# Kernel optimization log

Measured on AMD Instinct MI355X. Metric: run time of the kernel, lower is better.

Reference implementation:

```python
import jax, jax.numpy as jnp
import numpy as np

EPS = 1e-5

def _ln(x, g, b):
    mu = jnp.mean(x, axis=-1, keepdims=True)
    var = jnp.mean((x - mu) ** 2, axis=-1, keepdims=True)
    return (x - mu) / jnp.sqrt(var + EPS) * g + b

def setup_inputs() -> dict:
    key = jax.random.key(0)
    ks = jax.random.split(key, 8)
    S, B, L, M, D, Nq, H = 4, 256, 256, 4, 512, 4, 2048
    G = (M + 2) * D
    inp = {
        'ns_tokens': jax.random.normal(ks[0], (B, M, D), jnp.float32),
        'seq_tokens': jax.random.normal(ks[1], (S, B, L, D), jnp.float32),
        'seq_padding_masks': jax.random.randint(ks[2], (S, B, L), 0, 2).astype(bool),
        'seq_stats': jax.random.normal(ks[3], (S, B, 6), jnp.float32),
        'gin_gamma': jnp.ones((G,), jnp.float32),
        'gin_beta': jnp.zeros((G,), jnp.float32),
        'stat_W': 0.02 * jax.random.normal(ks[4], (S, 6, D), jnp.float32),
        'stat_b': jnp.zeros((S, D), jnp.float32),
        'stat_ln_g': jnp.ones((S, D), jnp.float32),
        'stat_ln_b': jnp.zeros((S, D), jnp.float32),
        'W1': 0.02 * jax.random.normal(ks[5], (S, Nq, G, H), jnp.float32),
        'b1': jnp.zeros((S, Nq, H), jnp.float32),
        'W2': 0.02 * jax.random.normal(ks[6], (S, Nq, H, D), jnp.float32),
        'b2': jnp.zeros((S, Nq, D), jnp.float32),
        'ln_g': jnp.ones((S, Nq, D), jnp.float32),
        'ln_b': jnp.zeros((S, Nq, D), jnp.float32),
    }
    return inp

def reference(ns_tokens, seq_tokens, seq_padding_masks, seq_stats,
              gin_gamma, gin_beta, stat_W, stat_b, stat_ln_g, stat_ln_b,
              W1, b1, W2, b2, ln_g, ln_b):
    S, B = seq_tokens.shape[0], ns_tokens.shape[0]
    ns_flat = ns_tokens.reshape(B, -1)                       # (B, M*D)
    valid = (~seq_padding_masks).astype(seq_tokens.dtype)[..., None]  # (S,B,L,1)
    denom = jnp.clip(jnp.sum(valid, axis=2), 1.0)            # (S,B,1)
    pooled = jnp.sum(seq_tokens * valid, axis=2) / denom     # (S,B,D)
    stat = jnp.einsum('sbf,sfd->sbd', seq_stats, stat_W) + stat_b[:, None]
    stat = _ln(stat, stat_ln_g[:, None], stat_ln_b[:, None])  # (S,B,D)
    gi = jnp.concatenate([jnp.broadcast_to(ns_flat[None], (S, B, ns_flat.shape[1])), pooled, stat], axis=-1)
    gi = _ln(gi, gin_gamma, gin_beta)                        # (S,B,G)
    h = jax.nn.silu(jnp.einsum('sbg,sqgh->sqbh', gi, W1) + b1[:, :, None])
    q = jnp.einsum('sqbh,sqhd->sqbd', h, W2) + b2[:, :, None]
    q = _ln(q, ln_g[:, :, None], ln_b[:, :, None])           # (S,Nq,B,D)
    return jnp.transpose(q, (0, 2, 1, 3))                    # (S,B,Nq,D)
```

## Files before the change

### kernel.cpp

```cpp
#include <hip/hip_runtime.h>
#include <hip/hip_bf16.h>

#define S_ 4
#define B_ 256
#define L_ 256
#define D_ 512
#define NQ_ 4
#define H_ 2048
#define G_ 3072

typedef __attribute__((ext_vector_type(4))) float f32x4;
typedef __attribute__((ext_vector_type(8))) short s16x8;

__device__ __forceinline__ unsigned short f2bf(float x) {
    __hip_bfloat16 hb = __float2bfloat16(x);
    return reinterpret_cast<unsigned short&>(hb);
}

__device__ __forceinline__ void gll16(const void* g, void* l) {
    __builtin_amdgcn_global_load_lds(
        (const __attribute__((address_space(1))) unsigned int*)g,
        (__attribute__((address_space(3))) unsigned int*)l, 16, 0, 0);
}

__device__ __forceinline__ float block_sum256(float v, float* red) {
    #pragma unroll
    for (int off = 32; off > 0; off >>= 1) v += __shfl_down(v, off, 64);
    int tid = threadIdx.x;
    int lane = tid & 63, wid = tid >> 6;
    if (lane == 0) red[wid] = v;
    __syncthreads();
    float r = (tid < 4) ? red[tid] : 0.f;
    #pragma unroll
    for (int off = 4; off > 0; off >>= 1) r += __shfl_down(r, off, 64);
    if (tid == 0) red[0] = r;
    __syncthreads();
    float out = red[0];
    __syncthreads();
    return out;
}

__global__ __launch_bounds__(256) void pool_kernel(
    const float* __restrict__ seq_tokens,
    const unsigned char* __restrict__ masks_raw,
    float* __restrict__ pooled)
{
    const int sb = blockIdx.x;
    const int tid = threadIdx.x;
    __shared__ float sval[L_];
    __shared__ float scount[4];
    __shared__ f32x4 spart[256];
    __shared__ int is_bool_flag;

    if (tid == 0) is_bool_flag = 0;
    __syncthreads();
    {
        unsigned int w = reinterpret_cast<const unsigned int*>(masks_raw)[tid];
        if (w & 0xFFFFFF00u) is_bool_flag = 1;
    }
    __syncthreads();
    const bool is_bool = (is_bool_flag != 0);

    int mval;
    if (is_bool) mval = masks_raw[(size_t)sb * L_ + tid];
    else         mval = reinterpret_cast<const int*>(masks_raw)[(size_t)sb * L_ + tid];
    float valid = mval ? 0.f : 1.f;
    sval[tid] = valid;
    float c = valid;
    #pragma unroll
    for (int off = 32; off > 0; off >>= 1) c += __shfl_down(c, off, 64);
    if ((tid & 63) == 0) scount[tid >> 6] = c;
    __syncthreads();
    const float denom = fmaxf(scount[0] + scount[1] + scount[2] + scount[3], 1.f);

    const float* base = seq_tokens + (size_t)sb * L_ * D_;
    const int cidx = tid & 127;
    const int rg = tid >> 7;
    f32x4 acc = {0.f, 0.f, 0.f, 0.f};
    for (int l = rg; l < L_; l += 2) {
        float vl = sval[l];
        f32x4 v = *reinterpret_cast<const f32x4*>(base + (size_t)l * D_ + cidx * 4);
        acc += v * vl;
    }
    spart[tid] = acc;
    __syncthreads();
    if (tid < 128) {
        f32x4 r = spart[tid] + spart[tid + 128];
        r *= (1.f / denom);
        *reinterpret_cast<f32x4*>(pooled + (size_t)sb * D_ + cidx * 4) = r;
    }
}

__global__ __launch_bounds__(256) void gi_kernel(
    const float* __restrict__ ns_tokens,
    const float* __restrict__ seq_stats,
    const float* __restrict__ stat_W,
    const float* __restrict__ stat_b,
    const float* __restrict__ stat_ln_g,
    const float* __restrict__ stat_ln_b,
    const float* __restrict__ gin_gamma,
    const float* __restrict__ gin_beta,
    const float* __restrict__ pooled,
    __hip_bfloat16* __restrict__ gi)
{
    const int sb = blockIdx.x;
    const int s = sb >> 8;
    const int b = sb & 255;
    const int tid = threadIdx.x;
    __shared__ float red[8];
    __shared__ float sstat[D_];

    float st[6];
    #pragma unroll
    for (int f = 0; f < 6; ++f) st[f] = seq_stats[(size_t)sb * 6 + f];

    float sp[2];
    #pragma unroll
    for (int k = 0; k < 2; ++k) {
        int d = tid + k * 256;
        float a = stat_b[s * D_ + d];
        #pragma unroll
        for (int f = 0; f < 6; ++f) a += st[f] * stat_W[(s * 6 + f) * D_ + d];
        sp[k] = a;
    }
    float ssum = block_sum256(sp[0] + sp[1], red);
    float ssq  = block_sum256(sp[0] * sp[0] + sp[1] * sp[1], red);
    float mu = ssum / D_;
    float var = ssq / D_ - mu * mu;
    float rinv = rsqrtf(var + 1e-5f);
    #pragma unroll
    for (int k = 0; k < 2; ++k) {
        int d = tid + k * 256;
        sstat[d] = (sp[k] - mu) * rinv * stat_ln_g[s * D_ + d] + stat_ln_b[s * D_ + d];
    }
    __syncthreads();

    float gv[12];
    float gsum = 0.f, gsq = 0.f;
    #pragma unroll
    for (int k = 0; k < 12; ++k) {
        int g = tid + k * 256;
        float v;
        if (g < 2048)       v = ns_tokens[(size_t)b * 2048 + g];
        else if (g < 2560)  v = pooled[(size_t)sb * D_ + (g - 2048)];
        else                v = sstat[g - 2560];
        gv[k] = v;
        gsum += v;
        gsq += v * v;
    }
    gsum = block_sum256(gsum, red);
    gsq  = block_sum256(gsq, red);
    mu = gsum / G_;
    var = gsq / G_ - mu * mu;
    rinv = rsqrtf(var + 1e-5f);
    #pragma unroll
    for (int k = 0; k < 12; ++k) {
        int g = tid + k * 256;
        float o = (gv[k] - mu) * rinv * gin_gamma[g] + gin_beta[g];
        gi[(size_t)sb * G_ + g] = __float2bfloat16(o);
    }
}

__global__ __launch_bounds__(256) void gemm1_kernel(
    const __hip_bfloat16* __restrict__ gi,
    const float* __restrict__ W1,
    const float* __restrict__ b1,
    __hip_bfloat16* __restrict__ hbuf)
{
    const int bid = blockIdx.x;
    const int wg = (bid & 7) * 64 + (bid >> 3);
    const int ntile = wg & 31;
    const int sq = wg >> 5;
    const int s = sq >> 2;
    const int tid = threadIdx.x;
    const int lane = tid & 63;
    const int wid = tid >> 6;

    __shared__ __align__(16) unsigned short As[2][256 * 64];
    __shared__ __align__(16) unsigned short Ws[2][64 * 64];

    const char* Ag = reinterpret_cast<const char*>(gi + (size_t)s * B_ * G_);
    const float* Wb = W1 + (size_t)sq * G_ * H_ + ntile * 64;

    f32x4 acc[4][4];
    #pragma unroll
    for (int i = 0; i < 4; ++i)
        #pragma unroll
        for (int j = 0; j < 4; ++j) acc[i][j] = (f32x4){0.f, 0.f, 0.f, 0.f};

    unsigned aoff[8];
    #pragma unroll
    for (int i = 0; i < 8; ++i) {
        int row = wid * 64 + i * 8 + (lane >> 3);
        int swz = ((lane >> 3) ^ i) & 7;
        aoff[i] = (unsigned)row * (G_ * 2) + (((lane & 7) ^ swz) * 16);
    }

    const int wn0 = (tid & 15) * 4;
    const int wk0 = (tid >> 4) * 4;
    unsigned offW[4];
    #pragma unroll
    for (int nn = 0; nn < 4; ++nn) {
        int row = wn0 + nn;
        int swz = (row ^ (row >> 3)) & 7;
        offW[nn] = (unsigned)((row * 128 + wk0 * 2) ^ (swz << 4));
    }

    unsigned offA[2][4], offB[2][4];
    #pragma unroll
    for (int kb = 0; kb < 2; ++kb) {
        #pragma unroll
        for (int mi = 0; mi < 4; ++mi) {
            int r = wid * 64 + mi * 16 + (lane & 15);
            int swz = (r ^ (r >> 3)) & 7;
            offA[kb][mi] = r * 128 + ((((lane >> 4) + kb * 4) ^ swz) * 16);
        }
        #pragma unroll
        for (int ni = 0; ni < 4; ++ni) {
            int r = ni * 16 + (lane & 15);
            int swz = (r ^ (r >> 3)) & 7;
            offB[kb][ni] = r * 128 + ((((lane >> 4) + kb * 4) ^ swz) * 16);
        }
    }

    {
        char* dst = reinterpret_cast<char*>(&As[0][0]);
        #pragma unroll
        for (int i = 0; i < 8; ++i)
            gll16(Ag + aoff[i], dst + (wid * 64 + i * 8) * 128);
        f32x4 w0[4];
        #pragma unroll
        for (int kk = 0; kk < 4; ++kk)
            w0[kk] = *reinterpret_cast<const f32x4*>(Wb + (size_t)(wk0 + kk) * H_ + wn0);
        #pragma unroll
        for (int nn = 0; nn < 4; ++nn) {
            unsigned long long pk =
                (unsigned long long)f2bf(w0[0][nn]) |
                ((unsigned long long)f2bf(w0[1][nn]) << 16) |
                ((unsigned long long)f2bf(w0[2][nn]) << 32) |
                ((unsigned long long)f2bf(w0[3][nn]) << 48);
            *reinterpret_cast<unsigned long long*>(reinterpret_cast<char*>(&Ws[0][0]) + offW[nn]) = pk;
        }
        asm volatile("s_waitcnt lgkmcnt(0)" ::: "memory");
        __builtin_amdgcn_s_barrier();
    }

    for (int kt = 0; kt < G_ / 64; ++kt) {
        const int cur = kt & 1, nxt = cur ^ 1;
        const int kn = (kt < G_ / 64 - 1) ? kt + 1 : G_ / 64 - 1;

        f32x4 wreg[4];
        {
            const float* wp = Wb + (size_t)(kn * 64 + wk0) * H_ + wn0;
            #pragma unroll
            for (int kk = 0; kk < 4; ++kk)
                wreg[kk] = *reinterpret_cast<const f32x4*>(wp + (size_t)kk * H_);
        }
        {
            char* dst = reinterpret_cast<char*>(&As[nxt][0]);
            const unsigned kbyte = (unsigned)kn * 128;
            #pragma unroll
            for (int i = 0; i < 8; ++i)
                gll16(Ag + (aoff[i] + kbyte), dst + (wid * 64 + i * 8) * 128);
        }
        asm volatile("s_waitcnt vmcnt(12)" ::: "memory");
        __builtin_amdgcn_sched_barrier(0);

        const char* Al = reinterpret_cast<const char*>(&As[cur][0]);
        const char* Wl = reinterpret_cast<const char*>(&Ws[cur][0]);
        #pragma unroll
        for (int kb = 0; kb < 2; ++kb) {
            s16x8 af[4], bfr[4];
            #pragma unroll
            for (int mi = 0; mi < 4; ++mi)
                af[mi] = *reinterpret_cast<const s16x8*>(Al + offA[kb][mi]);
            #pragma unroll
            for (int ni = 0; ni < 4; ++ni)
                bfr[ni] = *reinterpret_cast<const s16x8*>(Wl + offB[kb][ni]);
            #pragma unroll
            for (int mi = 0; mi < 4; ++mi)
                #pragma unroll
                for (int ni = 0; ni < 4; ++ni)
                    acc[mi][ni] = __builtin_amdgcn_mfma_f32_16x16x32_bf16(af[mi], bfr[ni], acc[mi][ni], 0, 0, 0);
        }

        #pragma unroll
        for (int nn = 0; nn < 4; ++nn) {
            unsigned long long pk =
                (unsigned long long)f2bf(wreg[0][nn]) |
                ((unsigned long long)f2bf(wreg[1][nn]) << 16) |
                ((unsigned long long)f2bf(wreg[2][nn]) << 32) |
                ((unsigned long long)f2bf(wreg[3][nn]) << 48);
            *reinterpret_cast<unsigned long long*>(reinterpret_cast<char*>(&Ws[nxt][0]) + offW[nn]) = pk;
        }
        asm volatile("s_waitcnt lgkmcnt(0)" ::: "memory");
        __builtin_amdgcn_s_barrier();
    }

    const float* b1p = b1 + (size_t)sq * H_ + ntile * 64;
    __hip_bfloat16* hp = hbuf + (size_t)sq * B_ * H_;
    #pragma unroll
    for (int mi = 0; mi < 4; ++mi)
        #pragma unroll
        for (int ni = 0; ni < 4; ++ni)
            #pragma unroll
            for (int r = 0; r < 4; ++r) {
                int row = wid * 64 + mi * 16 + ((lane >> 4) << 2) + r;
                int coll = ni * 16 + (lane & 15);
                float x = acc[mi][ni][r] + b1p[coll];
                float sg = 1.f / (1.f + __expf(-x));
                hp[(size_t)row * H_ + ntile * 64 + coll] = __float2bfloat16(x * sg);
            }
}

__global__ __launch_bounds__(256) void gemm2_kernel(
    const __hip_bfloat16* __restrict__ hbuf,
    const float* __restrict__ W2,
    __hip_bfloat16* __restrict__ qpre)
{
    const int bid = blockIdx.x;
    const int wg = (bid & 7) * 32 + (bid >> 3);
    const int ntile = wg & 7;
    const int mtile = (wg >> 3) & 1;
    const int sq = wg >> 4;
    const int tid = threadIdx.x;
    const int lane = tid & 63;
    const int wid = tid >> 6;
    const int wm = wid >> 1, wn = wid & 1;

    __shared__ __align__(16) unsigned short As[128 * 64];
    __shared__ __align__(16) unsigned short Ws[64 * 64];

    const __hip_bfloat16* Ab = hbuf + ((size_t)sq * B_ + mtile * 128) * H_;
    const float* Wb = W2 + (size_t)sq * H_ * D_ + ntile * 64;

    f32x4 acc[4][2];
    #pragma unroll
    for (int i = 0; i < 4; ++i)
        #pragma unroll
        for (int j = 0; j < 2; ++j) acc[i][j] = (f32x4){0.f, 0.f, 0.f, 0.f};

    const int wn0 = (tid & 15) * 4;
    const int wk0 = (tid >> 4) * 4;

    for (int kt = 0; kt < H_ / 64; ++kt) {
        const int kbase = kt * 64;
        __syncthreads();
        float wv[4][4];
        #pragma unroll
        for (int kk = 0; kk < 4; ++kk) {
            f32x4 t = *reinterpret_cast<const f32x4*>(Wb + (size_t)(kbase + wk0 + kk) * D_ + wn0);
            #pragma unroll
            for (int j = 0; j < 4; ++j) wv[kk][j] = t[j];
        }
        #pragma unroll
        for (int i = 0; i < 4; ++i) {
            int slot = i * 256 + tid;
            int row = slot >> 3, cc = slot & 7;
            int swz = (row ^ (row >> 3)) & 7;
            s16x8 v = *reinterpret_cast<const s16x8*>(Ab + (size_t)row * H_ + kbase + cc * 8);
            *reinterpret_cast<s16x8*>(&As[row * 64 + ((cc ^ swz) * 8)]) = v;
        }
        #pragma unroll
        for (int nn = 0; nn < 4; ++nn) {
            int row = wn0 + nn;
            int swz = (row ^ (row >> 3)) & 7;
            unsigned long long pk =
                (unsigned long long)f2bf(wv[0][nn]) |
                ((unsigned long long)f2bf(wv[1][nn]) << 16) |
                ((unsigned long long)f2bf(wv[2][nn]) << 32) |
                ((unsigned long long)f2bf(wv[3][nn]) << 48);
            int byteoff = (row * 128 + wk0 * 2) ^ (swz << 4);
            *reinterpret_cast<unsigned long long*>(reinterpret_cast<char*>(Ws) + byteoff) = pk;
        }
        __syncthreads();
        #pragma unroll
        for (int kb = 0; kb < 2; ++kb) {
            s16x8 af[4], bfr[2];
            #pragma unroll
            for (int mi = 0; mi < 4; ++mi) {
                int r = wm * 64 + mi * 16 + (lane & 15);
                int swz = (r ^ (r >> 3)) & 7;
                int chunk = ((lane >> 4) + kb * 4) ^ swz;
                af[mi] = *reinterpret_cast<const s16x8*>(&As[r * 64 + chunk * 8]);
            }
            #pragma unroll
            for (int ni = 0; ni < 2; ++ni) {
                int r = wn * 32 + ni * 16 + (lane & 15);
                int swz = (r ^ (r >> 3)) & 7;
                int chunk = ((lane >> 4) + kb * 4) ^ swz;
                bfr[ni] = *reinterpret_cast<const s16x8*>(&Ws[r * 64 + chunk * 8]);
            }
            #pragma unroll
            for (int mi = 0; mi < 4; ++mi)
                #pragma unroll
                for (int ni = 0; ni < 2; ++ni)
                    acc[mi][ni] = __builtin_amdgcn_mfma_f32_16x16x32_bf16(af[mi], bfr[ni], acc[mi][ni], 0, 0, 0);
        }
    }
    #pragma unroll
    for (int mi = 0; mi < 4; ++mi)
        #pragma unroll
        for (int ni = 0; ni < 2; ++ni)
            #pragma unroll
            for (int r = 0; r < 4; ++r) {
                int row = mtile * 128 + wm * 64 + mi * 16 + ((lane >> 4) << 2) + r;
                int col = ntile * 64 + wn * 32 + ni * 16 + (lane & 15);
                qpre[((size_t)sq * B_ + row) * D_ + col] = __float2bfloat16(acc[mi][ni][r]);
            }
}

__global__ __launch_bounds__(256) void lnout_kernel(
    const __hip_bfloat16* __restrict__ qpre,
    const float* __restrict__ b2,
    const float* __restrict__ lng,
    const float* __restrict__ lnb,
    float* __restrict__ out)
{
    const int idx = blockIdx.x;
    const int sq = idx >> 8;
    const int b = idx & 255;
    const int tid = threadIdx.x;
    __shared__ float red[8];

    float v[2];
    #pragma unroll
    for (int k = 0; k < 2; ++k) {
        int d = tid + k * 256;
        v[k] = __bfloat162float(qpre[(size_t)idx * D_ + d]) + b2[sq * D_ + d];
    }
    float sum = block_sum256(v[0] + v[1], red);
    float sq2 = block_sum256(v[0] * v[0] + v[1] * v[1], red);
    float mu = sum / D_;
    float var = sq2 / D_ - mu * mu;
    float rinv = rsqrtf(var + 1e-5f);
    const int s = sq >> 2, q = sq & 3;
    #pragma unroll
    for (int k = 0; k < 2; ++k) {
        int d = tid + k * 256;
        float o = (v[k] - mu) * rinv * lng[sq * D_ + d] + lnb[sq * D_ + d];
        out[(((size_t)s * B_ + b) * NQ_ + q) * D_ + d] = o;
    }
}

extern "C" void kernel_launch(void* const* d_in, const int* in_sizes, int n_in,
                              void* d_out, int out_size, void* d_ws, size_t ws_size,
                              hipStream_t stream) {
    const float* ns_tokens   = (const float*)d_in[0];
    const float* seq_tokens  = (const float*)d_in[1];
    const unsigned char* masks = (const unsigned char*)d_in[2];
    const float* seq_stats   = (const float*)d_in[3];
    const float* gin_gamma   = (const float*)d_in[4];
    const float* gin_beta    = (const float*)d_in[5];
    const float* stat_W      = (const float*)d_in[6];
    const float* stat_b      = (const float*)d_in[7];
    const float* stat_ln_g   = (const float*)d_in[8];
    const float* stat_ln_b   = (const float*)d_in[9];
    const float* W1          = (const float*)d_in[10];
    const float* b1          = (const float*)d_in[11];
    const float* W2          = (const float*)d_in[12];
    const float* b2          = (const float*)d_in[13];
    const float* ln_g        = (const float*)d_in[14];
    const float* ln_b        = (const float*)d_in[15];
    float* out = (float*)d_out;

    char* ws = (char*)d_ws;
    float* pooled        = (float*)(ws);
    __hip_bfloat16* gi   = (__hip_bfloat16*)(ws + 2097152);
    __hip_bfloat16* hbuf = (__hip_bfloat16*)(ws + 2097152 + 6291456);
    __hip_bfloat16* qpre = (__hip_bfloat16*)(ws + 2097152 + 6291456 + 16777216);

    pool_kernel<<<dim3(S_ * B_), dim3(256), 0, stream>>>(seq_tokens, masks, pooled);
    gi_kernel<<<dim3(S_ * B_), dim3(256), 0, stream>>>(ns_tokens, seq_stats, stat_W, stat_b,
                                                       stat_ln_g, stat_ln_b, gin_gamma, gin_beta,
                                                       pooled, gi);
    gemm1_kernel<<<dim3(32 * S_ * NQ_), dim3(256), 0, stream>>>(gi, W1, b1, hbuf);
    gemm2_kernel<<<dim3(2 * D_ / 64 * S_ * NQ_), dim3(256), 0, stream>>>(hbuf, W2, qpre);
    lnout_kernel<<<dim3(S_ * NQ_ * B_), dim3(256), 0, stream>>>(qpre, b2, ln_g, ln_b, out);
}
```

Measured before the change: 268.8 us.

## Prefetch W1 fp32 tiles two k-steps ahead with register double-buffering in gemm1

The gemm1 main loop now holds two register sets for the fp32 W1 tile and issues the global load for tile k+2 while tile k+1 is converted to bf16 and written to LDS before the MFMAs. The loop is unrolled by two with a macro so the register roles alternate. This is meant to hide the global-memory latency of the W1 stream, which previously had only one iteration of slack. In exchange, each thread holds sixteen more registers, which may reduce occupancy, and the LDS conversion store now sits before the MFMA block instead of after it.

```diff
diff --git a/kernel.cpp b/kernel.cpp
--- a/kernel.cpp
+++ b/kernel.cpp
@@ -161,6 +161,55 @@
     }
 }
 
+#define G1_BODY(KT, CUR, NXT, WP, WQ)                                                  \
+  {                                                                                    \
+    const int kn2 = ((KT) < 46) ? (KT) + 2 : 47;                                       \
+    const float* wp_ = Wb + (size_t)(kn2 * 64 + wk0) * H_ + wn0;                       \
+    _Pragma("unroll")                                                                  \
+    for (int kk = 0; kk < 4; ++kk)                                                     \
+        WQ[kk] = *reinterpret_cast<const f32x4*>(wp_ + (size_t)kk * H_);               \
+    {                                                                                  \
+        const int kn1 = ((KT) < 47) ? (KT) + 1 : 47;                                   \
+        char* dst = reinterpret_cast<char*>(&As[NXT][0]);                              \
+        const unsigned kbyte = (unsigned)kn1 * 128;                                    \
+        _Pragma("unroll")                                                              \
+        for (int i = 0; i < 8; ++i)                                                    \
+            gll16(Ag + (aoff[i] + kbyte), dst + (wid * 64 + i * 8) * 128);             \
+    }                                                                                  \
+    asm volatile("s_waitcnt vmcnt(12)" ::: "memory");                                  \
+    __builtin_amdgcn_sched_barrier(0);                                                 \
+    _Pragma("unroll")                                                                  \
+    for (int nn = 0; nn < 4; ++nn) {                                                   \
+        unsigned long long pk =                                                        \
+            (unsigned long long)f2bf(WP[0][nn]) |                                      \
+            ((unsigned long long)f2bf(WP[1][nn]) << 16) |                              \
+            ((unsigned long long)f2bf(WP[2][nn]) << 32) |                              \
+            ((unsigned long long)f2bf(WP[3][nn]) << 48);                               \
+        *reinterpret_cast<unsigned long long*>(                                        \
+            reinterpret_cast<char*>(&Ws[NXT][0]) + offW[nn]) = pk;                     \
+    }                                                                                  \
+    const char* Al = reinterpret_cast<const char*>(&As[CUR][0]);                       \
+    const char* Wl = reinterpret_cast<const char*>(&Ws[CUR][0]);                       \
+    _Pragma("unroll")                                                                  \
+    for (int kb = 0; kb < 2; ++kb) {                                                   \
+        s16x8 af[4], bfr[4];                                                           \
+        _Pragma("unroll")                                                              \
+        for (int mi = 0; mi < 4; ++mi)                                                 \
+            af[mi] = *reinterpret_cast<const s16x8*>(Al + offA[kb][mi]);               \
+        _Pragma("unroll")                                                              \
+        for (int ni = 0; ni < 4; ++ni)                                                 \
+            bfr[ni] = *reinterpret_cast<const s16x8*>(Wl + offB[kb][ni]);              \
+        _Pragma("unroll")                                                              \
+        for (int mi = 0; mi < 4; ++mi)                                                 \
+            _Pragma("unroll")                                                          \
+            for (int ni = 0; ni < 4; ++ni)                                             \
+                acc[mi][ni] = __builtin_amdgcn_mfma_f32_16x16x32_bf16(                 \
+                    af[mi], bfr[ni], acc[mi][ni], 0, 0, 0);                            \
+    }                                                                                  \
+    asm volatile("s_waitcnt lgkmcnt(0)" ::: "memory");                                 \
+    __builtin_amdgcn_s_barrier();                                                      \
+  }
+
 __global__ __launch_bounds__(256) void gemm1_kernel(
     const __hip_bfloat16* __restrict__ gi,
     const float* __restrict__ W1,
@@ -223,78 +272,38 @@
         }
     }
 
+    f32x4 wA[4], wB[4];
+
     {
         char* dst = reinterpret_cast<char*>(&As[0][0]);
         #pragma unroll
         for (int i = 0; i < 8; ++i)
             gll16(Ag + aoff[i], dst + (wid * 64 + i * 8) * 128);
-        f32x4 w0[4];
         #pragma unroll
         for (int kk = 0; kk < 4; ++kk)
-            w0[kk] = *reinterpret_cast<const f32x4*>(Wb + (size_t)(wk0 + kk) * H_ + wn0);
+            wA[kk] = *reinterpret_cast<const f32x4*>(Wb + (size_t)(wk0 + kk) * H_ + wn0);
+        const float* wp1 = Wb + (size_t)(64 + wk0) * H_ + wn0;
+        #pragma unroll
+        for (int kk = 0; kk < 4; ++kk)
+            wB[kk] = *reinterpret_cast<const f32x4*>(wp1 + (size_t)kk * H_);
+        asm volatile("s_waitcnt vmcnt(4)" ::: "memory");
+        __builtin_amdgcn_sched_barrier(0);
         #pragma unroll
         for (int nn = 0; nn < 4; ++nn) {
             unsigned long long pk =
-                (unsigned long long)f2bf(w0[0][nn]) |
-                ((unsigned long long)f2bf(w0[1][nn]) << 16) |
-                ((unsigned long long)f2bf(w0[2][nn]) << 32) |
-                ((unsigned long long)f2bf(w0[3][nn]) << 48);
+                (unsigned long long)f2bf(wA[0][nn]) |
+                ((unsigned long long)f2bf(wA[1][nn]) << 16) |
+                ((unsigned long long)f2bf(wA[2][nn]) << 32) |
+                ((unsigned long long)f2bf(wA[3][nn]) << 48);
             *reinterpret_cast<unsigned long long*>(reinterpret_cast<char*>(&Ws[0][0]) + offW[nn]) = pk;
         }
         asm volatile("s_waitcnt lgkmcnt(0)" ::: "memory");
         __builtin_amdgcn_s_barrier();
     }
 
-    for (int kt = 0; kt < G_ / 64; ++kt) {
-        const int cur = kt & 1, nxt = cur ^ 1;
-        const int kn = (kt < G_ / 64 - 1) ? kt + 1 : G_ / 64 - 1;
-
-        f32x4 wreg[4];
-        {
-            const float* wp = Wb + (size_t)(kn * 64 + wk0) * H_ + wn0;
-            #pragma unroll
-            for (int kk = 0; kk < 4; ++kk)
-                wreg[kk] = *reinterpret_cast<const f32x4*>(wp + (size_t)kk * H_);
-        }
-        {
-            char* dst = reinterpret_cast<char*>(&As[nxt][0]);
-            const unsigned kbyte = (unsigned)kn * 128;
-            #pragma unroll
-            for (int i = 0; i < 8; ++i)
-                gll16(Ag + (aoff[i] + kbyte), dst + (wid * 64 + i * 8) * 128);
-        }
-        asm volatile("s_waitcnt vmcnt(12)" ::: "memory");
-        __builtin_amdgcn_sched_barrier(0);
-
-        const char* Al = reinterpret_cast<const char*>(&As[cur][0]);
-        const char* Wl = reinterpret_cast<const char*>(&Ws[cur][0]);
-        #pragma unroll
-        for (int kb = 0; kb < 2; ++kb) {
-            s16x8 af[4], bfr[4];
-            #pragma unroll
-            for (int mi = 0; mi < 4; ++mi)
-                af[mi] = *reinterpret_cast<const s16x8*>(Al + offA[kb][mi]);
-            #pragma unroll
-            for (int ni = 0; ni < 4; ++ni)
-                bfr[ni] = *reinterpret_cast<const s16x8*>(Wl + offB[kb][ni]);
-            #pragma unroll
-            for (int mi = 0; mi < 4; ++mi)
-                #pragma unroll
-                for (int ni = 0; ni < 4; ++ni)
-                    acc[mi][ni] = __builtin_amdgcn_mfma_f32_16x16x32_bf16(af[mi], bfr[ni], acc[mi][ni], 0, 0, 0);
-        }
-
-        #pragma unroll
-        for (int nn = 0; nn < 4; ++nn) {
-            unsigned long long pk =
-                (unsigned long long)f2bf(wreg[0][nn]) |
-                ((unsigned long long)f2bf(wreg[1][nn]) << 16) |
-                ((unsigned long long)f2bf(wreg[2][nn]) << 32) |
-                ((unsigned long long)f2bf(wreg[3][nn]) << 48);
-            *reinterpret_cast<unsigned long long*>(reinterpret_cast<char*>(&Ws[nxt][0]) + offW[nn]) = pk;
-        }
-        asm volatile("s_waitcnt lgkmcnt(0)" ::: "memory");
-        __builtin_amdgcn_s_barrier();
+    for (int kt = 0; kt < 48; kt += 2) {
+        G1_BODY(kt,     0, 1, wB, wA);
+        G1_BODY(kt + 1, 1, 0, wA, wB);
     }
 
     const float* b1p = b1 + (size_t)sq * H_ + ntile * 64;
```

After: 310.6 us. 1.16x slower.

## Double-buffer gemm2 with async LDS loads and narrower N tiles for more blocks

Applied to the files above, without the earlier changes.

Rewrites the second GEMM so the hbuf tile goes straight from global memory into LDS with global_load_lds into a double buffer. The next W2 tile is loaded into registers while the current tile runs MFMAs, and only one barrier is taken per K step. The N tile shrinks from 64 to 32 columns, doubling the grid to 512 blocks for better CU coverage, and launch bounds request 4 blocks per CU. The cost is that each block reuses less A data, so hbuf is read from global memory twice as often, and correctness now depends on the hand-written waitcnt placement.

```diff
diff --git a/kernel.cpp b/kernel.cpp
--- a/kernel.cpp
+++ b/kernel.cpp
@@ -313,99 +313,141 @@
             }
 }
 
-__global__ __launch_bounds__(256) void gemm2_kernel(
+__global__ __launch_bounds__(256, 4) void gemm2_kernel(
     const __hip_bfloat16* __restrict__ hbuf,
     const float* __restrict__ W2,
     __hip_bfloat16* __restrict__ qpre)
 {
     const int bid = blockIdx.x;
-    const int wg = (bid & 7) * 32 + (bid >> 3);
-    const int ntile = wg & 7;
-    const int mtile = (wg >> 3) & 1;
-    const int sq = wg >> 4;
+    const int wg = (bid & 7) * 64 + (bid >> 3);
+    const int ntile = wg & 15;
+    const int mtile = (wg >> 4) & 1;
+    const int sq = wg >> 5;
     const int tid = threadIdx.x;
     const int lane = tid & 63;
     const int wid = tid >> 6;
-    const int wm = wid >> 1, wn = wid & 1;
-
-    __shared__ __align__(16) unsigned short As[128 * 64];
-    __shared__ __align__(16) unsigned short Ws[64 * 64];
-
-    const __hip_bfloat16* Ab = hbuf + ((size_t)sq * B_ + mtile * 128) * H_;
-    const float* Wb = W2 + (size_t)sq * H_ * D_ + ntile * 64;
-
-    f32x4 acc[4][2];
-    #pragma unroll
-    for (int i = 0; i < 4; ++i)
+
+    __shared__ __align__(16) unsigned short As[2][128 * 64];
+    __shared__ __align__(16) unsigned short Ws[2][32 * 64];
+
+    const char* Ag = reinterpret_cast<const char*>(hbuf + ((size_t)sq * B_ + mtile * 128) * H_);
+    const float* Wb = W2 + (size_t)sq * H_ * D_ + ntile * 32;
+
+    f32x4 acc[2][2];
+    #pragma unroll
+    for (int i = 0; i < 2; ++i)
         #pragma unroll
         for (int j = 0; j < 2; ++j) acc[i][j] = (f32x4){0.f, 0.f, 0.f, 0.f};
 
-    const int wn0 = (tid & 15) * 4;
-    const int wk0 = (tid >> 4) * 4;
+    unsigned aoff[4];
+    #pragma unroll
+    for (int i = 0; i < 4; ++i) {
+        int row = wid * 32 + i * 8 + (lane >> 3);
+        int swz = ((lane >> 3) ^ (row >> 3)) & 7;
+        aoff[i] = (unsigned)row * (H_ * 2) + (((lane & 7) ^ swz) * 16);
+    }
+
+    const int wn0 = (tid & 7) * 4;
+    const int wk0 = (tid >> 3) * 2;
+    unsigned offW[4];
+    #pragma unroll
+    for (int nn = 0; nn < 4; ++nn) {
+        int row = wn0 + nn;
+        int swz = (row ^ (row >> 3)) & 7;
+        offW[nn] = (unsigned)((row * 128 + wk0 * 2) ^ (swz << 4));
+    }
+
+    unsigned offA[2][2], offB[2][2];
+    #pragma unroll
+    for (int kb = 0; kb < 2; ++kb) {
+        #pragma unroll
+        for (int mi = 0; mi < 2; ++mi) {
+            int r = wid * 32 + mi * 16 + (lane & 15);
+            int swz = (r ^ (r >> 3)) & 7;
+            offA[kb][mi] = r * 128 + ((((lane >> 4) + kb * 4) ^ swz) * 16);
+        }
+        #pragma unroll
+        for (int ni = 0; ni < 2; ++ni) {
+            int r = ni * 16 + (lane & 15);
+            int swz = (r ^ (r >> 3)) & 7;
+            offB[kb][ni] = r * 128 + ((((lane >> 4) + kb * 4) ^ swz) * 16);
+        }
+    }
+
+    {
+        char* dst = reinterpret_cast<char*>(&As[0][0]);
+        #pragma unroll
+        for (int i = 0; i < 4; ++i)
+            gll16(Ag + aoff[i], dst + (wid * 32 + i * 8) * 128);
+        f32x4 w0[2];
+        #pragma unroll
+        for (int kk = 0; kk < 2; ++kk)
+            w0[kk] = *reinterpret_cast<const f32x4*>(Wb + (size_t)(wk0 + kk) * D_ + wn0);
+        #pragma unroll
+        for (int nn = 0; nn < 4; ++nn) {
+            unsigned pk = (unsigned)f2bf(w0[0][nn]) | ((unsigned)f2bf(w0[1][nn]) << 16);
+            *reinterpret_cast<unsigned*>(reinterpret_cast<char*>(&Ws[0][0]) + offW[nn]) = pk;
+        }
+        asm volatile("s_waitcnt lgkmcnt(0)" ::: "memory");
+        __builtin_amdgcn_s_barrier();
+    }
 
     for (int kt = 0; kt < H_ / 64; ++kt) {
-        const int kbase = kt * 64;
-        __syncthreads();
-        float wv[4][4];
-        #pragma unroll
-        for (int kk = 0; kk < 4; ++kk) {
-            f32x4 t = *reinterpret_cast<const f32x4*>(Wb + (size_t)(kbase + wk0 + kk) * D_ + wn0);
-            #pragma unroll
-            for (int j = 0; j < 4; ++j) wv[kk][j] = t[j];
-        }
-        #pragma unroll
-        for (int i = 0; i < 4; ++i) {
-            int slot = i * 256 + tid;
-            int row = slot >> 3, cc = slot & 7;
-            int swz = (row ^ (row >> 3)) & 7;
-            s16x8 v = *reinterpret_cast<const s16x8*>(Ab + (size_t)row * H_ + kbase + cc * 8);
-            *reinterpret_cast<s16x8*>(&As[row * 64 + ((cc ^ swz) * 8)]) = v;
-        }
-        #pragma unroll
-        for (int nn = 0; nn < 4; ++nn) {
-            int row = wn0 + nn;
-            int swz = (row ^ (row >> 3)) & 7;
-            unsigned long long pk =
-                (unsigned long long)f2bf(wv[0][nn]) |
-                ((unsigned long long)f2bf(wv[1][nn]) << 16) |
-                ((unsigned long long)f2bf(wv[2][nn]) << 32) |
-                ((unsigned long long)f2bf(wv[3][nn]) << 48);
-            int byteoff = (row * 128 + wk0 * 2) ^ (swz << 4);
-            *reinterpret_cast<unsigned long long*>(reinterpret_cast<char*>(Ws) + byteoff) = pk;
-        }
-        __syncthreads();
+        const int cur = kt & 1, nxt = cur ^ 1;
+        const int kn = (kt < H_ / 64 - 1) ? kt + 1 : H_ / 64 - 1;
+
+        f32x4 wreg[2];
+        {
+            const float* wp = Wb + (size_t)(kn * 64 + wk0) * D_ + wn0;
+            #pragma unroll
+            for (int kk = 0; kk < 2; ++kk)
+                wreg[kk] = *reinterpret_cast<const f32x4*>(wp + (size_t)kk * D_);
+        }
+        {
+            char* dst = reinterpret_cast<char*>(&As[nxt][0]);
+            const unsigned kbyte = (unsigned)kn * 128;
+            #pragma unroll
+            for (int i = 0; i < 4; ++i)
+                gll16(Ag + (aoff[i] + kbyte), dst + (wid * 32 + i * 8) * 128);
+        }
+        asm volatile("s_waitcnt vmcnt(6)" ::: "memory");
+        __builtin_amdgcn_sched_barrier(0);
+
+        const char* Al = reinterpret_cast<const char*>(&As[cur][0]);
+        const char* Wl = reinterpret_cast<const char*>(&Ws[cur][0]);
         #pragma unroll
         for (int kb = 0; kb < 2; ++kb) {
-            s16x8 af[4], bfr[2];
-            #pragma unroll
-            for (int mi = 0; mi < 4; ++mi) {
-                int r = wm * 64 + mi * 16 + (lane & 15);
-                int swz = (r ^ (r >> 3)) & 7;
-                int chunk = ((lane >> 4) + kb * 4) ^ swz;
-                af[mi] = *reinterpret_cast<const s16x8*>(&As[r * 64 + chunk * 8]);
-            }
-            #pragma unroll
-            for (int ni = 0; ni < 2; ++ni) {
-                int r = wn * 32 + ni * 16 + (lane & 15);
-                int swz = (r ^ (r >> 3)) & 7;
-                int chunk = ((lane >> 4) + kb * 4) ^ swz;
-                bfr[ni] = *reinterpret_cast<const s16x8*>(&Ws[r * 64 + chunk * 8]);
-            }
-            #pragma unroll
-            for (int mi = 0; mi < 4; ++mi)
+            s16x8 af[2], bfr[2];
+            #pragma unroll
+            for (int mi = 0; mi < 2; ++mi)
+                af[mi] = *reinterpret_cast<const s16x8*>(Al + offA[kb][mi]);
+            #pragma unroll
+            for (int ni = 0; ni < 2; ++ni)
+                bfr[ni] = *reinterpret_cast<const s16x8*>(Wl + offB[kb][ni]);
+            #pragma unroll
+            for (int mi = 0; mi < 2; ++mi)
                 #pragma unroll
                 for (int ni = 0; ni < 2; ++ni)
                     acc[mi][ni] = __builtin_amdgcn_mfma_f32_16x16x32_bf16(af[mi], bfr[ni], acc[mi][ni], 0, 0, 0);
         }
-    }
-    #pragma unroll
-    for (int mi = 0; mi < 4; ++mi)
+
+        #pragma unroll
+        for (int nn = 0; nn < 4; ++nn) {
+            unsigned pk = (unsigned)f2bf(wreg[0][nn]) | ((unsigned)f2bf(wreg[1][nn]) << 16);
+            *reinterpret_cast<unsigned*>(reinterpret_cast<char*>(&Ws[nxt][0]) + offW[nn]) = pk;
+        }
+        asm volatile("s_waitcnt lgkmcnt(0)" ::: "memory");
+        __builtin_amdgcn_s_barrier();
+    }
+
+    #pragma unroll
+    for (int mi = 0; mi < 2; ++mi)
         #pragma unroll
         for (int ni = 0; ni < 2; ++ni)
             #pragma unroll
             for (int r = 0; r < 4; ++r) {
-                int row = mtile * 128 + wm * 64 + mi * 16 + ((lane >> 4) << 2) + r;
-                int col = ntile * 64 + wn * 32 + ni * 16 + (lane & 15);
+                int row = mtile * 128 + wid * 32 + mi * 16 + ((lane >> 4) << 2) + r;
+                int col = ntile * 32 + ni * 16 + (lane & 15);
                 qpre[((size_t)sq * B_ + row) * D_ + col] = __float2bfloat16(acc[mi][ni][r]);
             }
 }
@@ -475,6 +517,6 @@
                                                        stat_ln_g, stat_ln_b, gin_gamma, gin_beta,
                                                        pooled, gi);
     gemm1_kernel<<<dim3(32 * S_ * NQ_), dim3(256), 0, stream>>>(gi, W1, b1, hbuf);
-    gemm2_kernel<<<dim3(2 * D_ / 64 * S_ * NQ_), dim3(256), 0, stream>>>(hbuf, W2, qpre);
+    gemm2_kernel<<<dim3(512), dim3(256), 0, stream>>>(hbuf, W2, qpre);
     lnout_kernel<<<dim3(S_ * NQ_ * B_), dim3(256), 0, stream>>>(qpre, b2, ln_g, ln_b, out);
 }
```

Measured after the change: 266.3 us. No clear change (-0.9%).
